# Kernel optimization log

Hardware: AMD Instinct MI355X
Metric: run time of the kernel (lower is better)

Reference implementation:

```python
import jax, jax.numpy as jnp
import numpy as np

N_NODES = 100_000
N_EDGES = 1_600_000
HID = 64
TXT = 384
N_LAYERS = 2
BATCH = 1024


def setup_inputs() -> dict:
    key = jax.random.key(0)
    ks = jax.random.split(key, 13)
    s = 0.05
    return {
        "text_emb": jax.random.normal(ks[0], (N_NODES, TXT), dtype=jnp.float32),
        "weights": jax.random.uniform(ks[1], (N_EDGES,), dtype=jnp.float32),
        "W_enc": jax.random.normal(ks[2], (TXT, HID), dtype=jnp.float32) * s,
        "b_enc": jax.random.normal(ks[3], (HID,), dtype=jnp.float32) * s,
        "Wself_f": jax.random.normal(ks[4], (N_LAYERS, HID, HID), dtype=jnp.float32) * s,
        "Wneigh_f": jax.random.normal(ks[5], (N_LAYERS, HID, HID), dtype=jnp.float32) * s,
        "b_f": jax.random.normal(ks[6], (N_LAYERS, HID), dtype=jnp.float32) * s,
        "Wself_r": jax.random.normal(ks[7], (N_LAYERS, HID, HID), dtype=jnp.float32) * s,
        "Wneigh_r": jax.random.normal(ks[8], (N_LAYERS, HID, HID), dtype=jnp.float32) * s,
        "b_r": jax.random.normal(ks[9], (N_LAYERS, HID), dtype=jnp.float32) * s,
        "src": jax.random.randint(ks[10], (N_EDGES,), 0, N_NODES, dtype=jnp.int32),
        "dst": jax.random.randint(ks[11], (N_EDGES,), 0, N_NODES, dtype=jnp.int32),
        "ids_idx": jax.random.randint(ks[12], (BATCH,), 0, N_NODES, dtype=jnp.int32),
    }


def _inv_degree(idx, n, e_dtype):
    deg = jax.ops.segment_sum(jnp.ones((idx.shape[0],), dtype=e_dtype), idx, num_segments=n)
    return jnp.where(deg > 0, 1.0 / deg, 0.0)  # zero in-degree -> 0 (DGL mean)


def _sage_mean(x, src, dst, w, inv_deg, Wself, Wneigh, b):
    # DGL SAGEConv('mean') with edge_weight: neigh = mean_over_in_edges(w * h_src)
    m = w[:, None] * x[src]                                   # [E, H] gather
    neigh = jax.ops.segment_sum(m, dst, num_segments=x.shape[0]) * inv_deg[:, None]
    return x @ Wself + neigh @ Wneigh + b


def reference(text_emb, weights, W_enc, b_enc, Wself_f, Wneigh_f, b_f,
              Wself_r, Wneigh_r, b_r, src, dst, ids_idx):
    n = text_emb.shape[0]
    inv_f = _inv_degree(dst, n, text_emb.dtype)   # forward graph: aggregate into dst
    inv_r = _inv_degree(src, n, text_emb.dtype)   # reversed graph: aggregate into src
    x = text_emb @ W_enc + b_enc                  # text encoder
    for l in range(Wself_f.shape[0]):
        y = jax.nn.relu(_sage_mean(x, src, dst, weights, inv_f,
                                   Wself_f[l], Wneigh_f[l], b_f[l]))
        y = y + jax.nn.relu(_sage_mean(x, dst, src, weights, inv_r,
                                       Wself_r[l], Wneigh_r[l], b_r[l]))
        x = x + y                                 # skip connection
    feat = x[ids_idx]                             # [B, H]
    return feat / jnp.linalg.norm(feat, axis=1, keepdims=True)
```

## Files before the change

### kernel.cpp

```cpp
#include <hip/hip_runtime.h>

#define NN 100000
#define NE 1600000
#define HID 64
#define TXT 384
#define BATCH 1024
#define NBUCK 391
#define SBLK 256
#define EPB ((NE + SBLK - 1) / SBLK)
#define LDA 40
#define LDK2 72

typedef __attribute__((ext_vector_type(8))) short short8;
typedef __attribute__((ext_vector_type(4))) float float4v;

__device__ __forceinline__ ushort f2bf(float f) {
  unsigned u = __float_as_uint(f);
  unsigned r = (u + 0x7fffu + ((u >> 16) & 1u)) >> 16;
  return (ushort)r;
}
__device__ __forceinline__ float bf2f(ushort u) {
  return __uint_as_float(((unsigned)u) << 16);
}
__device__ __forceinline__ short8 pack8(float4 a, float4 b) {
  short8 s;
  s[0] = (short)f2bf(a.x); s[1] = (short)f2bf(a.y);
  s[2] = (short)f2bf(a.z); s[3] = (short)f2bf(a.w);
  s[4] = (short)f2bf(b.x); s[5] = (short)f2bf(b.y);
  s[6] = (short)f2bf(b.z); s[7] = (short)f2bf(b.w);
  return s;
}

__global__ void k_hist2(const int* __restrict__ src, const int* __restrict__ dst,
                        int* __restrict__ cm_f, int* __restrict__ cm_r,
                        int* __restrict__ flagz) {
  __shared__ int hf[NBUCK], hr[NBUCK];
  const int t = threadIdx.x, blk = blockIdx.x;
  const int gid = blk * 256 + t;
  if (gid < NN / 4) flagz[gid] = 0;
  for (int i = t; i < NBUCK; i += 256) { hf[i] = 0; hr[i] = 0; }
  __syncthreads();
  const int e0 = blk * EPB, e1 = min(NE, e0 + EPB);
  for (int e = e0 + t; e < e1; e += 256) {
    atomicAdd(&hf[dst[e] >> 8], 1);
    atomicAdd(&hr[src[e] >> 8], 1);
  }
  __syncthreads();
  for (int i = t; i < NBUCK; i += 256) {
    cm_f[i * SBLK + blk] = hf[i];
    cm_r[i * SBLK + blk] = hr[i];
  }
}

__global__ void k_scan1(int* __restrict__ cm_f, int* __restrict__ cm_r,
                        int* __restrict__ btot) {
  __shared__ int tmp[256];
  const int t = threadIdx.x;
  int b = blockIdx.x;
  int* cm = (b < NBUCK) ? cm_f : cm_r;
  int bucket = (b < NBUCK) ? b : b - NBUCK;
  int* row = cm + bucket * SBLK;
  int v = row[t];
  tmp[t] = v; __syncthreads();
  for (int d = 1; d < 256; d <<= 1) {
    int s = tmp[t]; if (t >= d) s += tmp[t - d];
    __syncthreads(); tmp[t] = s; __syncthreads();
  }
  row[t] = tmp[t] - v;
  if (t == 255) btot[b] = tmp[t];
}

__global__ void k_scan2(const int* __restrict__ btot,
                        int* __restrict__ bbase_f, int* __restrict__ bbase_r) {
  __shared__ int tmp[512];
  const int t = threadIdx.x;
  int h = (t < NBUCK) ? btot[t] : 0;
  tmp[t] = h; __syncthreads();
  for (int d = 1; d < 512; d <<= 1) {
    int v = tmp[t]; if (t >= d) v += tmp[t - d];
    __syncthreads(); tmp[t] = v; __syncthreads();
  }
  if (t < NBUCK) bbase_f[t] = tmp[t] - h;
  __syncthreads();
  h = (t < NBUCK) ? btot[NBUCK + t] : 0;
  tmp[t] = h; __syncthreads();
  for (int d = 1; d < 512; d <<= 1) {
    int v = tmp[t]; if (t >= d) v += tmp[t - d];
    __syncthreads(); tmp[t] = v; __syncthreads();
  }
  if (t < NBUCK) bbase_r[t] = tmp[t] - h;
}

__global__ void k_scatter2(const int* __restrict__ src, const int* __restrict__ dst,
                           const float* __restrict__ w,
                           const int* __restrict__ cm_f, const int* __restrict__ cm_r,
                           const int* __restrict__ bbase_f, const int* __restrict__ bbase_r,
                           int2* __restrict__ stg_f, int2* __restrict__ stg_r) {
  __shared__ int cur_f[NBUCK], cur_r[NBUCK];
  const int t = threadIdx.x, blk = blockIdx.x;
  for (int i = t; i < NBUCK; i += 256) {
    cur_f[i] = bbase_f[i] + cm_f[i * SBLK + blk];
    cur_r[i] = bbase_r[i] + cm_r[i * SBLK + blk];
  }
  __syncthreads();
  const int e0 = blk * EPB, e1 = min(NE, e0 + EPB);
  for (int e = e0 + t; e < e1; e += 256) {
    int s = src[e], d = dst[e];
    int wb = __float_as_int(w[e]);
    int p = atomicAdd(&cur_f[d >> 8], 1);
    stg_f[p] = make_int2(((d & 255) << 24) | s, wb);
    int q = atomicAdd(&cur_r[s >> 8], 1);
    stg_r[q] = make_int2(((s & 255) << 24) | d, wb);
  }
}

__global__ void p_build(const int2* __restrict__ stgf, const int* __restrict__ btotf,
                        const int* __restrict__ bbasef,
                        int* __restrict__ startf, int* __restrict__ cntf,
                        int2* __restrict__ cvf, int* __restrict__ permf,
                        const int2* __restrict__ stgr, const int* __restrict__ btotr,
                        const int* __restrict__ bbaser,
                        int* __restrict__ startr, int* __restrict__ cntr,
                        int2* __restrict__ cvr, int* __restrict__ permr) {
  int b = blockIdx.x;
  const int2* stg; const int* bcnt; const int* bbase;
  int* start; int* cnt; int2* cv; int* perm;
  if (b < NBUCK) { stg = stgf; bcnt = btotf; bbase = bbasef; start = startf; cnt = cntf; cv = cvf; perm = permf; }
  else { b -= NBUCK; stg = stgr; bcnt = btotr; bbase = bbaser; start = startr; cnt = cntr; cv = cvr; perm = permr; }
  const int base = bbase[b];
  const int n = bcnt[b];
  const int t = threadIdx.x;
  __shared__ int hist[256], tmp[256], cur[256], dh[256], dc[256];
  hist[t] = 0;
  perm[b * 256 + t] = -1;
  __syncthreads();
  for (int i = t; i < n; i += 256) {
    unsigned pk = (unsigned)stg[base + i].x;
    atomicAdd(&hist[pk >> 24], 1);
  }
  __syncthreads();
  const int h = hist[t];
  tmp[t] = h; __syncthreads();
  for (int d = 1; d < 256; d <<= 1) {
    int v = tmp[t]; if (t >= d) v += tmp[t - d];
    __syncthreads(); tmp[t] = v; __syncthreads();
  }
  const int excl = tmp[t] - h;
  const int node = (b << 8) + t;
  const bool valid = (node < NN);
  if (valid) { start[node] = base + excl; cnt[node] = h; }
  cur[t] = excl;
  dh[t] = 0; __syncthreads();
  const int dcap = min(h, 255);
  if (valid) atomicAdd(&dh[dcap], 1);
  __syncthreads();
  int dv = dh[t];
  tmp[t] = dv; __syncthreads();
  for (int d = 1; d < 256; d <<= 1) {
    int v = tmp[t]; if (t >= d) v += tmp[t - d];
    __syncthreads(); tmp[t] = v; __syncthreads();
  }
  dc[t] = tmp[t] - dv;
  __syncthreads();
  if (valid) {
    int pos = atomicAdd(&dc[dcap], 1);
    perm[b * 256 + pos] = node;
  }
  __syncthreads();
  for (int i = t; i < n; i += 256) {
    int2 en = stg[base + i];
    unsigned d8 = ((unsigned)en.x) >> 24;
    int pos = atomicAdd(&cur[d8], 1);
    cv[base + pos] = make_int2(en.x & 0xFFFFFF, en.y);
  }
}

__global__ void k_flag(const int* __restrict__ ids,
                       const int* __restrict__ startf, const int* __restrict__ cntf,
                       const int2* __restrict__ cvf,
                       const int* __restrict__ startr, const int* __restrict__ cntr,
                       const int2* __restrict__ cvr,
                       unsigned char* __restrict__ flag) {
  int b = blockIdx.x * 256 + threadIdx.x;
  if (b >= BATCH) return;
  int row = ids[b];
  flag[row] = 1;
  int s = startf[row], e = s + cntf[row];
  for (int j = s; j < e; ++j) flag[cvf[j].x] = 1;
  s = startr[row]; e = s + cntr[row];
  for (int j = s; j < e; ++j) flag[cvr[j].x] = 1;
}

__global__ void k_gather3(const ushort* __restrict__ xb,
                          const unsigned char* __restrict__ flag,
                          const int* __restrict__ permf, const int* __restrict__ startf,
                          const int* __restrict__ cntf, const int2* __restrict__ cvf,
                          ushort* __restrict__ nbf,
                          const int* __restrict__ permr, const int* __restrict__ startr,
                          const int* __restrict__ cntr, const int2* __restrict__ cvr,
                          ushort* __restrict__ nbr) {
  const int BPD = (NBUCK * 256) / 16;
  int b = blockIdx.x;
  const int *perm, *start, *cnt; const int2* cv; ushort* outp;
  if (b < BPD) { perm = permf; start = startf; cnt = cntf; cv = cvf; outp = nbf; }
  else { b -= BPD; perm = permr; start = startr; cnt = cntr; cv = cvr; outp = nbr; }
  const int lane = threadIdx.x & 63;
  const int wave = threadIdx.x >> 6;
  const int slot = b * 16 + wave * 4 + (lane >> 4);
  const int fl = (lane & 15) * 4;
  const int row = perm[slot];
  if (row < 0) return;
  if (!flag[row]) return;
  const int s = start[row], c = cnt[row];
  const int e = s + c;
  float a0 = 0.f, a1 = 0.f, a2 = 0.f, a3 = 0.f;
  int j = s;
  for (; j + 4 <= e; j += 4) {
    int2 e0 = cv[j], e1 = cv[j + 1], e2 = cv[j + 2], e3 = cv[j + 3];
    uint2 v0 = *(const uint2*)(xb + (size_t)e0.x * 64 + fl);
    uint2 v1 = *(const uint2*)(xb + (size_t)e1.x * 64 + fl);
    uint2 v2 = *(const uint2*)(xb + (size_t)e2.x * 64 + fl);
    uint2 v3 = *(const uint2*)(xb + (size_t)e3.x * 64 + fl);
    float w0 = __int_as_float(e0.y), w1 = __int_as_float(e1.y);
    float w2 = __int_as_float(e2.y), w3 = __int_as_float(e3.y);
    a0 += w0 * bf2f((ushort)v0.x); a1 += w0 * bf2f((ushort)(v0.x >> 16));
    a2 += w0 * bf2f((ushort)v0.y); a3 += w0 * bf2f((ushort)(v0.y >> 16));
    a0 += w1 * bf2f((ushort)v1.x); a1 += w1 * bf2f((ushort)(v1.x >> 16));
    a2 += w1 * bf2f((ushort)v1.y); a3 += w1 * bf2f((ushort)(v1.y >> 16));
    a0 += w2 * bf2f((ushort)v2.x); a1 += w2 * bf2f((ushort)(v2.x >> 16));
    a2 += w2 * bf2f((ushort)v2.y); a3 += w2 * bf2f((ushort)(v2.y >> 16));
    a0 += w3 * bf2f((ushort)v3.x); a1 += w3 * bf2f((ushort)(v3.x >> 16));
    a2 += w3 * bf2f((ushort)v3.y); a3 += w3 * bf2f((ushort)(v3.y >> 16));
  }
  for (; j < e; ++j) {
    int2 ee = cv[j];
    uint2 v = *(const uint2*)(xb + (size_t)ee.x * 64 + fl);
    float ww = __int_as_float(ee.y);
    a0 += ww * bf2f((ushort)v.x); a1 += ww * bf2f((ushort)(v.x >> 16));
    a2 += ww * bf2f((ushort)v.y); a3 += ww * bf2f((ushort)(v.y >> 16));
  }
  float inv = (c > 0) ? 1.0f / (float)c : 0.f;
  uint2 pv;
  pv.x = (uint)f2bf(a0 * inv) | ((uint)f2bf(a1 * inv) << 16);
  pv.y = (uint)f2bf(a2 * inv) | ((uint)f2bf(a3 * inv) << 16);
  *(uint2*)(outp + (size_t)row * 64 + fl) = pv;
}

__global__ void k_bgather(const ushort* __restrict__ xb, const int* __restrict__ ids,
                          const int* __restrict__ startf, const int* __restrict__ cntf,
                          const int2* __restrict__ cvf, ushort* __restrict__ nbf,
                          const int* __restrict__ startr, const int* __restrict__ cntr,
                          const int2* __restrict__ cvr, ushort* __restrict__ nbr) {
  const int lane = threadIdx.x & 63;
  const int wave = threadIdx.x >> 6;
  const int fl = (lane & 15) * 4;
  const int t = blockIdx.x * 16 + wave * 4 + (lane >> 4);
  const int rev = (t >= BATCH);
  const int b = rev ? t - BATCH : t;
  const int row = ids[b];
  const int* start = rev ? startr : startf;
  const int* cnt   = rev ? cntr   : cntf;
  const int2* cv   = rev ? cvr    : cvf;
  ushort* outp     = rev ? nbr    : nbf;
  const int s = start[row], c = cnt[row];
  const int e = s + c;
  float a0 = 0.f, a1 = 0.f, a2 = 0.f, a3 = 0.f;
  int j = s;
  for (; j + 4 <= e; j += 4) {
    int2 e0 = cv[j], e1 = cv[j + 1], e2 = cv[j + 2], e3 = cv[j + 3];
    uint2 v0 = *(const uint2*)(xb + (size_t)e0.x * 64 + fl);
    uint2 v1 = *(const uint2*)(xb + (size_t)e1.x * 64 + fl);
    uint2 v2 = *(const uint2*)(xb + (size_t)e2.x * 64 + fl);
    uint2 v3 = *(const uint2*)(xb + (size_t)e3.x * 64 + fl);
    float w0 = __int_as_float(e0.y), w1 = __int_as_float(e1.y);
    float w2 = __int_as_float(e2.y), w3 = __int_as_float(e3.y);
    a0 += w0 * bf2f((ushort)v0.x); a1 += w0 * bf2f((ushort)(v0.x >> 16));
    a2 += w0 * bf2f((ushort)v0.y); a3 += w0 * bf2f((ushort)(v0.y >> 16));
    a0 += w1 * bf2f((ushort)v1.x); a1 += w1 * bf2f((ushort)(v1.x >> 16));
    a2 += w1 * bf2f((ushort)v1.y); a3 += w1 * bf2f((ushort)(v1.y >> 16));
    a0 += w2 * bf2f((ushort)v2.x); a1 += w2 * bf2f((ushort)(v2.x >> 16));
    a2 += w2 * bf2f((ushort)v2.y); a3 += w2 * bf2f((ushort)(v2.y >> 16));
    a0 += w3 * bf2f((ushort)v3.x); a1 += w3 * bf2f((ushort)(v3.x >> 16));
    a2 += w3 * bf2f((ushort)v3.y); a3 += w3 * bf2f((ushort)(v3.y >> 16));
  }
  for (; j < e; ++j) {
    int2 ee = cv[j];
    uint2 v = *(const uint2*)(xb + (size_t)ee.x * 64 + fl);
    float ww = __int_as_float(ee.y);
    a0 += ww * bf2f((ushort)v.x); a1 += ww * bf2f((ushort)(v.x >> 16));
    a2 += ww * bf2f((ushort)v.y); a3 += ww * bf2f((ushort)(v.y >> 16));
  }
  float inv = (c > 0) ? 1.0f / (float)c : 0.f;
  uint2 pv;
  pv.x = (uint)f2bf(a0 * inv) | ((uint)f2bf(a1 * inv) << 16);
  pv.y = (uint)f2bf(a2 * inv) | ((uint)f2bf(a3 * inv) << 16);
  *(uint2*)(outp + (size_t)b * 64 + fl) = pv;
}

__global__ void k_wtile(const float* __restrict__ W, ushort* __restrict__ Wt) {
  int b = blockIdx.x;
  int ch = b >> 2, nt = b & 3;
  int lane = threadIdx.x;
  int quad = lane >> 4, lr = lane & 15;
  short8 s;
  #pragma unroll
  for (int j = 0; j < 8; ++j)
    s[j] = (short)f2bf(W[(ch * 32 + quad * 8 + j) * 64 + nt * 16 + lr]);
  *(short8*)&Wt[((size_t)b * 64 + lane) * 8] = s;
}

__launch_bounds__(256)
__global__ void k_enc3(const float* __restrict__ T, const ushort* __restrict__ Wt,
                       const float* __restrict__ bias,
                       float* __restrict__ x, ushort* __restrict__ xb) {
  __shared__ short As[2][128 * LDA];
  const int tid = threadIdx.x;
  const int row0 = blockIdx.x * 128;
  const int wave = tid >> 6, lane = tid & 63;
  const int quad = lane >> 4, lr = lane & 15;
  const int srow = tid >> 1, shalf = (tid & 1) * 16;
  const int grow = min(row0 + srow, NN - 1);
  const float* tp = T + (size_t)grow * TXT + shalf;

  float4 pa0 = *(const float4*)(tp);
  float4 pa1 = *(const float4*)(tp + 4);
  float4 pa2 = *(const float4*)(tp + 8);
  float4 pa3 = *(const float4*)(tp + 12);
  *(short8*)&As[0][srow * LDA + shalf] = pack8(pa0, pa1);
  *(short8*)&As[0][srow * LDA + shalf + 8] = pack8(pa2, pa3);
  pa0 = *(const float4*)(tp + 32);
  pa1 = *(const float4*)(tp + 36);
  pa2 = *(const float4*)(tp + 40);
  pa3 = *(const float4*)(tp + 44);
  __syncthreads();

  const ushort* pw = Wt + lane * 8;
  float4v acc[2][4] = {};
  #pragma unroll
  for (int ch = 0; ch < 12; ++ch) {
    const short* Ac = As[ch & 1];
    short8 af0 = *(const short8*)&Ac[(wave * 32 + lr) * LDA + quad * 8];
    short8 af1 = *(const short8*)&Ac[(wave * 32 + 16 + lr) * LDA + quad * 8];
    #pragma unroll
    for (int nt = 0; nt < 4; ++nt) {
      short8 bfrag = *(const short8*)(pw + (size_t)(ch * 4 + nt) * 512);
      acc[0][nt] = __builtin_amdgcn_mfma_f32_16x16x32_bf16(af0, bfrag, acc[0][nt], 0, 0, 0);
      acc[1][nt] = __builtin_amdgcn_mfma_f32_16x16x32_bf16(af1, bfrag, acc[1][nt], 0, 0, 0);
    }
    if (ch < 11) {
      short* An = As[(ch + 1) & 1];
      *(short8*)&An[srow * LDA + shalf] = pack8(pa0, pa1);
      *(short8*)&An[srow * LDA + shalf + 8] = pack8(pa2, pa3);
      if (ch + 2 < 12) {
        const float* q = tp + (ch + 2) * 32;
        pa0 = *(const float4*)(q);
        pa1 = *(const float4*)(q + 4);
        pa2 = *(const float4*)(q + 8);
        pa3 = *(const float4*)(q + 12);
      }
      __syncthreads();
    }
  }
  #pragma unroll
  for (int nt = 0; nt < 4; ++nt) {
    const int col = nt * 16 + lr;
    const float bcol = bias[col];
    #pragma unroll
    for (int mt = 0; mt < 2; ++mt) {
      #pragma unroll
      for (int r = 0; r < 4; ++r) {
        const int row = row0 + wave * 32 + mt * 16 + quad * 4 + r;
        if (row < NN) {
          float v = acc[mt][nt][r] + bcol;
          x[(size_t)row * 64 + col] = v;
          xb[(size_t)row * 64 + col] = f2bf(v);
        }
      }
    }
  }
}

__launch_bounds__(256)
__global__ void k_layer(const ushort* __restrict__ xbin,
                        const ushort* __restrict__ nbf, const ushort* __restrict__ nbr,
                        const float* __restrict__ Wsf, const float* __restrict__ Wnf,
                        const float* __restrict__ bfv,
                        const float* __restrict__ Wsr, const float* __restrict__ Wnr,
                        const float* __restrict__ brv,
                        float* __restrict__ x, ushort* __restrict__ xb) {
  __shared__ short B4[4 * 64 * LDK2];
  __shared__ short As[128 * LDK2];
  const int tid = threadIdx.x;
  const int row0 = blockIdx.x * 128;
  const int wave = tid >> 6, lane = tid & 63;
  const int quad = lane >> 4, lr = lane & 15;

  {
    const float* wm0 = Wsf; const float* wm1 = Wsr;
    const float* wm2 = Wnf; const float* wm3 = Wnr;
    #pragma unroll
    for (int j = 0; j < 16; ++j) {
      int idx = j * 256 + tid;
      int k = idx >> 6, n = idx & 63;
      B4[0 * 64 * LDK2 + n * LDK2 + k] = (short)f2bf(wm0[idx]);
      B4[1 * 64 * LDK2 + n * LDK2 + k] = (short)f2bf(wm1[idx]);
      B4[2 * 64 * LDK2 + n * LDK2 + k] = (short)f2bf(wm2[idx]);
      B4[3 * 64 * LDK2 + n * LDK2 + k] = (short)f2bf(wm3[idx]);
    }
  }
  const int srow = tid >> 1, half = (tid & 1) * 32;
  const int grow = min(row0 + srow, NN - 1);
  {
    const uint4* s = (const uint4*)(xbin + (size_t)grow * 64 + half);
    uint4* d = (uint4*)&As[srow * LDK2 + half];
    d[0] = s[0]; d[1] = s[1]; d[2] = s[2]; d[3] = s[3];
  }
  const uint4* pf = (const uint4*)(nbf + (size_t)grow * 64 + half);
  uint4 p0 = pf[0], p1 = pf[1], p2 = pf[2], p3 = pf[3];
  __syncthreads();

  float4v accf[2][4] = {}, accr[2][4] = {};
  #pragma unroll
  for (int kk = 0; kk < 64; kk += 32) {
    short8 a0 = *(const short8*)&As[(wave * 32 + lr) * LDK2 + kk + quad * 8];
    short8 a1 = *(const short8*)&As[(wave * 32 + 16 + lr) * LDK2 + kk + quad * 8];
    #pragma unroll
    for (int nt = 0; nt < 4; ++nt) {
      short8 bs = *(const short8*)&B4[0 * 64 * LDK2 + (nt * 16 + lr) * LDK2 + kk + quad * 8];
      accf[0][nt] = __builtin_amdgcn_mfma_f32_16x16x32_bf16(a0, bs, accf[0][nt], 0, 0, 0);
      accf[1][nt] = __builtin_amdgcn_mfma_f32_16x16x32_bf16(a1, bs, accf[1][nt], 0, 0, 0);
      short8 bq = *(const short8*)&B4[1 * 64 * LDK2 + (nt * 16 + lr) * LDK2 + kk + quad * 8];
      accr[0][nt] = __builtin_amdgcn_mfma_f32_16x16x32_bf16(a0, bq, accr[0][nt], 0, 0, 0);
      accr[1][nt] = __builtin_amdgcn_mfma_f32_16x16x32_bf16(a1, bq, accr[1][nt], 0, 0, 0);
    }
  }
  __syncthreads();
  { uint4* d = (uint4*)&As[srow * LDK2 + half]; d[0] = p0; d[1] = p1; d[2] = p2; d[3] = p3; }
  {
    const uint4* pr = (const uint4*)(nbr + (size_t)grow * 64 + half);
    p0 = pr[0]; p1 = pr[1]; p2 = pr[2]; p3 = pr[3];
  }
  __syncthreads();
  #pragma unroll
  for (int kk = 0; kk < 64; kk += 32) {
    short8 a0 = *(const short8*)&As[(wave * 32 + lr) * LDK2 + kk + quad * 8];
    short8 a1 = *(const short8*)&As[(wave * 32 + 16 + lr) * LDK2 + kk + quad * 8];
    #pragma unroll
    for (int nt = 0; nt < 4; ++nt) {
      short8 bs = *(const short8*)&B4[2 * 64 * LDK2 + (nt * 16 + lr) * LDK2 + kk + quad * 8];
      accf[0][nt] = __builtin_amdgcn_mfma_f32_16x16x32_bf16(a0, bs, accf[0][nt], 0, 0, 0);
      accf[1][nt] = __builtin_amdgcn_mfma_f32_16x16x32_bf16(a1, bs, accf[1][nt], 0, 0, 0);
    }
  }
  __syncthreads();
  { uint4* d = (uint4*)&As[srow * LDK2 + half]; d[0] = p0; d[1] = p1; d[2] = p2; d[3] = p3; }
  __syncthreads();
  #pragma unroll
  for (int kk = 0; kk < 64; kk += 32) {
    short8 a0 = *(const short8*)&As[(wave * 32 + lr) * LDK2 + kk + quad * 8];
    short8 a1 = *(const short8*)&As[(wave * 32 + 16 + lr) * LDK2 + kk + quad * 8];
    #pragma unroll
    for (int nt = 0; nt < 4; ++nt) {
      short8 bs = *(const short8*)&B4[3 * 64 * LDK2 + (nt * 16 + lr) * LDK2 + kk + quad * 8];
      accr[0][nt] = __builtin_amdgcn_mfma_f32_16x16x32_bf16(a0, bs, accr[0][nt], 0, 0, 0);
      accr[1][nt] = __builtin_amdgcn_mfma_f32_16x16x32_bf16(a1, bs, accr[1][nt], 0, 0, 0);
    }
  }
  #pragma unroll
  for (int nt = 0; nt < 4; ++nt) {
    const int col = nt * 16 + lr;
    const float bf_c = bfv[col], br_c = brv[col];
    #pragma unroll
    for (int mt = 0; mt < 2; ++mt) {
      #pragma unroll
      for (int r = 0; r < 4; ++r) {
        const int row = row0 + wave * 32 + mt * 16 + quad * 4 + r;
        if (row < NN) {
          size_t idx = (size_t)row * 64 + col;
          float v = x[idx] + fmaxf(accf[mt][nt][r] + bf_c, 0.f)
                           + fmaxf(accr[mt][nt][r] + br_c, 0.f);
          x[idx] = v;
          xb[idx] = f2bf(v);
        }
      }
    }
  }
}

__launch_bounds__(256)
__global__ void k_blayer(const ushort* __restrict__ xbin, const float* __restrict__ x,
                         const int* __restrict__ ids,
                         const ushort* __restrict__ nbf, const ushort* __restrict__ nbr,
                         const float* __restrict__ Wsf, const float* __restrict__ Wnf,
                         const float* __restrict__ bfv,
                         const float* __restrict__ Wsr, const float* __restrict__ Wnr,
                         const float* __restrict__ brv,
                         float* __restrict__ out) {
  __shared__ short B4[4 * 64 * LDK2];
  __shared__ short As[128 * LDK2];
  const int tid = threadIdx.x;
  const int b0 = blockIdx.x * 128;
  const int wave = tid >> 6, lane = tid & 63;
  const int quad = lane >> 4, lr = lane & 15;

  #pragma unroll
  for (int j = 0; j < 16; ++j) {
    int idx = j * 256 + tid;
    int k = idx >> 6, n = idx & 63;
    B4[0 * 64 * LDK2 + n * LDK2 + k] = (short)f2bf(Wsf[idx]);
    B4[1 * 64 * LDK2 + n * LDK2 + k] = (short)f2bf(Wsr[idx]);
    B4[2 * 64 * LDK2 + n * LDK2 + k] = (short)f2bf(Wnf[idx]);
    B4[3 * 64 * LDK2 + n * LDK2 + k] = (short)f2bf(Wnr[idx]);
  }
  const int srow = tid >> 1, half = (tid & 1) * 32;
  const int node0 = ids[b0 + srow];
  {
    const uint4* s = (const uint4*)(xbin + (size_t)node0 * 64 + half);
    uint4* d = (uint4*)&As[srow * LDK2 + half];
    d[0] = s[0]; d[1] = s[1]; d[2] = s[2]; d[3] = s[3];
  }
  __syncthreads();

  float4v accf[2][4] = {}, accr[2][4] = {};
  #pragma unroll
  for (int kk = 0; kk < 64; kk += 32) {
    short8 a0 = *(const short8*)&As[(wave * 32 + lr) * LDK2 + kk + quad * 8];
    short8 a1 = *(const short8*)&As[(wave * 32 + 16 + lr) * LDK2 + kk + quad * 8];
    #pragma unroll
    for (int nt = 0; nt < 4; ++nt) {
      short8 bs = *(const short8*)&B4[0 * 64 * LDK2 + (nt * 16 + lr) * LDK2 + kk + quad * 8];
      accf[0][nt] = __builtin_amdgcn_mfma_f32_16x16x32_bf16(a0, bs, accf[0][nt], 0, 0, 0);
      accf[1][nt] = __builtin_amdgcn_mfma_f32_16x16x32_bf16(a1, bs, accf[1][nt], 0, 0, 0);
      short8 bq = *(const short8*)&B4[1 * 64 * LDK2 + (nt * 16 + lr) * LDK2 + kk + quad * 8];
      accr[0][nt] = __builtin_amdgcn_mfma_f32_16x16x32_bf16(a0, bq, accr[0][nt], 0, 0, 0);
      accr[1][nt] = __builtin_amdgcn_mfma_f32_16x16x32_bf16(a1, bq, accr[1][nt], 0, 0, 0);
    }
  }
  __syncthreads();
  {
    const uint4* s = (const uint4*)(nbf + (size_t)(b0 + srow) * 64 + half);
    uint4* d = (uint4*)&As[srow * LDK2 + half];
    d[0] = s[0]; d[1] = s[1]; d[2] = s[2]; d[3] = s[3];
  }
  __syncthreads();
  #pragma unroll
  for (int kk = 0; kk < 64; kk += 32) {
    short8 a0 = *(const short8*)&As[(wave * 32 + lr) * LDK2 + kk + quad * 8];
    short8 a1 = *(const short8*)&As[(wave * 32 + 16 + lr) * LDK2 + kk + quad * 8];
    #pragma unroll
    for (int nt = 0; nt < 4; ++nt) {
      short8 bs = *(const short8*)&B4[2 * 64 * LDK2 + (nt * 16 + lr) * LDK2 + kk + quad * 8];
      accf[0][nt] = __builtin_amdgcn_mfma_f32_16x16x32_bf16(a0, bs, accf[0][nt], 0, 0, 0);
      accf[1][nt] = __builtin_amdgcn_mfma_f32_16x16x32_bf16(a1, bs, accf[1][nt], 0, 0, 0);
    }
  }
  __syncthreads();
  {
    const uint4* s = (const uint4*)(nbr + (size_t)(b0 + srow) * 64 + half);
    uint4* d = (uint4*)&As[srow * LDK2 + half];
    d[0] = s[0]; d[1] = s[1]; d[2] = s[2]; d[3] = s[3];
  }
  __syncthreads();
  #pragma unroll
  for (int kk = 0; kk < 64; kk += 32) {
    short8 a0 = *(const short8*)&As[(wave * 32 + lr) * LDK2 + kk + quad * 8];
    short8 a1 = *(const short8*)&As[(wave * 32 + 16 + lr) * LDK2 + kk + quad * 8];
    #pragma unroll
    for (int nt = 0; nt < 4; ++nt) {
      short8 bs = *(const short8*)&B4[3 * 64 * LDK2 + (nt * 16 + lr) * LDK2 + kk + quad * 8];
      accr[0][nt] = __builtin_amdgcn_mfma_f32_16x16x32_bf16(a0, bs, accr[0][nt], 0, 0, 0);
      accr[1][nt] = __builtin_amdgcn_mfma_f32_16x16x32_bf16(a1, bs, accr[1][nt], 0, 0, 0);
    }
  }
  float vv[2][4][4];
  #pragma unroll
  for (int nt = 0; nt < 4; ++nt) {
    const int col = nt * 16 + lr;
    const float bf_c = bfv[col], br_c = brv[col];
    #pragma unroll
    for (int mt = 0; mt < 2; ++mt) {
      #pragma unroll
      for (int r = 0; r < 4; ++r) {
        const int rl = wave * 32 + mt * 16 + quad * 4 + r;
        const int node = ids[b0 + rl];
        vv[mt][nt][r] = x[(size_t)node * 64 + col]
                      + fmaxf(accf[mt][nt][r] + bf_c, 0.f)
                      + fmaxf(accr[mt][nt][r] + br_c, 0.f);
      }
    }
  }
  #pragma unroll
  for (int mt = 0; mt < 2; ++mt) {
    #pragma unroll
    for (int r = 0; r < 4; ++r) {
      float s = 0.f;
      #pragma unroll
      for (int nt = 0; nt < 4; ++nt) s += vv[mt][nt][r] * vv[mt][nt][r];
      s += __shfl_xor(s, 1); s += __shfl_xor(s, 2);
      s += __shfl_xor(s, 4); s += __shfl_xor(s, 8);
      const int rl = wave * 32 + mt * 16 + quad * 4 + r;
      const float inv = 1.f / sqrtf(s);
      #pragma unroll
      for (int nt = 0; nt < 4; ++nt)
        out[(size_t)(b0 + rl) * 64 + nt * 16 + lr] = vv[mt][nt][r] * inv;
    }
  }
}

extern "C" void kernel_launch(void* const* d_in, const int* in_sizes, int n_in,
                              void* d_out, int out_size, void* d_ws, size_t ws_size,
                              hipStream_t stream) {
  const float* text = (const float*)d_in[0];
  const float* wts  = (const float*)d_in[1];
  const float* Wenc = (const float*)d_in[2];
  const float* benc = (const float*)d_in[3];
  const float* Wsf  = (const float*)d_in[4];
  const float* Wnf  = (const float*)d_in[5];
  const float* bf   = (const float*)d_in[6];
  const float* Wsr  = (const float*)d_in[7];
  const float* Wnr  = (const float*)d_in[8];
  const float* br   = (const float*)d_in[9];
  const int*   src  = (const int*)d_in[10];
  const int*   dst  = (const int*)d_in[11];
  const int*   ids  = (const int*)d_in[12];
  float* out = (float*)d_out;

  char* ws = (char*)d_ws;
  size_t o = 0;
  auto alloc = [&](size_t f32elems) {
    void* p = ws + o;
    o += f32elems * 4;
    o = (o + 255) & ~(size_t)255;
    return p;
  };
  float*  x   = (float*)alloc((size_t)NN * 64);
  ushort* xb  = (ushort*)alloc((size_t)NN * 32);
  ushort* nbf = (ushort*)alloc((size_t)NN * 32);
  ushort* nbr = (ushort*)alloc((size_t)NN * 32);
  ushort* Wt  = (ushort*)alloc(48 * 512 / 2);
  int2*   cvf = (int2*)alloc((size_t)NE * 2);
  int2*   cvr = (int2*)alloc((size_t)NE * 2);
  int* cm_f    = (int*)alloc((size_t)NBUCK * SBLK);
  int* cm_r    = (int*)alloc((size_t)NBUCK * SBLK);
  int* btot    = (int*)alloc(2 * NBUCK);
  int* bbase_f = (int*)alloc(NBUCK);
  int* bbase_r = (int*)alloc(NBUCK);
  int* startf  = (int*)alloc(NN);
  int* cntf    = (int*)alloc(NN);
  int* startr  = (int*)alloc(NN);
  int* cntr    = (int*)alloc(NN);
  int* permf   = (int*)alloc((size_t)NBUCK * 256);
  int* permr   = (int*)alloc((size_t)NBUCK * 256);
  unsigned char* flag = (unsigned char*)alloc(NN / 4 + 64);

  int2* stg_f = (int2*)nbf;
  int2* stg_r = (int2*)nbr;

  const int EB2 = (NN + 127) / 128;

  k_wtile<<<48, 64, 0, stream>>>(Wenc, Wt);
  k_hist2<<<SBLK, 256, 0, stream>>>(src, dst, cm_f, cm_r, (int*)flag);
  k_scan1<<<2 * NBUCK, 256, 0, stream>>>(cm_f, cm_r, btot);
  k_scan2<<<1, 512, 0, stream>>>(btot, bbase_f, bbase_r);
  k_scatter2<<<SBLK, 256, 0, stream>>>(src, dst, wts, cm_f, cm_r,
                                       bbase_f, bbase_r, stg_f, stg_r);
  p_build<<<2 * NBUCK, 256, 0, stream>>>(stg_f, btot, bbase_f, startf, cntf, cvf, permf,
                                         stg_r, btot + NBUCK, bbase_r, startr, cntr, cvr, permr);
  k_flag<<<BATCH / 256, 256, 0, stream>>>(ids, startf, cntf, cvf, startr, cntr, cvr, flag);
  k_enc3<<<EB2, 256, 0, stream>>>(text, Wt, benc, x, xb);

  const int GB3 = 2 * ((NBUCK * 256) / 16);
  k_gather3<<<GB3, 256, 0, stream>>>(xb, flag, permf, startf, cntf, cvf, nbf,
                                     permr, startr, cntr, cvr, nbr);
  k_layer<<<EB2, 256, 0, stream>>>(xb, nbf, nbr,
                                   Wsf, Wnf, bf, Wsr, Wnr, br, x, xb);
  k_bgather<<<(2 * BATCH) / 16, 256, 0, stream>>>(xb, ids, startf, cntf, cvf, nbf,
                                                  startr, cntr, cvr, nbr);
  k_blayer<<<BATCH / 128, 256, 0, stream>>>(xb, x, ids, nbf, nbr,
                                            Wsf + HID * HID, Wnf + HID * HID, bf + HID,
                                            Wsr + HID * HID, Wnr + HID * HID, br + HID,
                                            out);
}
```

Baseline: 517.4 us.

## Prune CSR build and layer-1 work to the batch's one-hop neighbourhood

Computes the set of flagged nodes (batch nodes plus their in- and out-neighbours) up front with an extra pass over the edges. That set then filters the histogram, the scatter and the per-node CSR build, so only edges into flagged nodes are bucketed. The flagged rows are compacted into a list, and the first SAGE layer runs its MFMA update only over those rows instead of all nodes. This cuts scatter traffic and layer-1 compute, in exchange for an extra edge sweep with random byte lookups, an atomic compaction step, and indirect row indexing in the layer kernel.

```diff
diff --git a/kernel.cpp b/kernel.cpp
--- a/kernel.cpp
+++ b/kernel.cpp
@@ -31,19 +31,50 @@
   return s;
 }
 
+__global__ void k_clear(unsigned char* __restrict__ idmap,
+                        unsigned char* __restrict__ flag, int* __restrict__ nf) {
+  int i = blockIdx.x * 256 + threadIdx.x;
+  if (i < NN) { idmap[i] = 0; flag[i] = 0; }
+  if (i == 0) *nf = 0;
+}
+
+__global__ void k_seed(const int* __restrict__ ids,
+                       unsigned char* __restrict__ idmap,
+                       unsigned char* __restrict__ flag) {
+  int b = blockIdx.x * 256 + threadIdx.x;
+  if (b < BATCH) { int r = ids[b]; idmap[r] = 1; flag[r] = 1; }
+}
+
+__global__ void k_fedges(const int* __restrict__ src, const int* __restrict__ dst,
+                         const unsigned char* __restrict__ idmap,
+                         unsigned char* __restrict__ flag) {
+  const int t = threadIdx.x, blk = blockIdx.x;
+  const int e0 = blk * EPB, e1 = min(NE, e0 + EPB);
+  for (int e = e0 + t; e < e1; e += 256) {
+    int s = src[e], d = dst[e];
+    if (idmap[d]) flag[s] = 1;
+    if (idmap[s]) flag[d] = 1;
+  }
+}
+
+__global__ void k_compact(const unsigned char* __restrict__ flag,
+                          int* __restrict__ frows, int* __restrict__ nf) {
+  int i = blockIdx.x * 256 + threadIdx.x;
+  if (i < NN && flag[i]) frows[atomicAdd(nf, 1)] = i;
+}
+
 __global__ void k_hist2(const int* __restrict__ src, const int* __restrict__ dst,
-                        int* __restrict__ cm_f, int* __restrict__ cm_r,
-                        int* __restrict__ flagz) {
+                        const unsigned char* __restrict__ flag,
+                        int* __restrict__ cm_f, int* __restrict__ cm_r) {
   __shared__ int hf[NBUCK], hr[NBUCK];
   const int t = threadIdx.x, blk = blockIdx.x;
-  const int gid = blk * 256 + t;
-  if (gid < NN / 4) flagz[gid] = 0;
   for (int i = t; i < NBUCK; i += 256) { hf[i] = 0; hr[i] = 0; }
   __syncthreads();
   const int e0 = blk * EPB, e1 = min(NE, e0 + EPB);
   for (int e = e0 + t; e < e1; e += 256) {
-    atomicAdd(&hf[dst[e] >> 8], 1);
-    atomicAdd(&hr[src[e] >> 8], 1);
+    int s = src[e], d = dst[e];
+    if (flag[d]) atomicAdd(&hf[d >> 8], 1);
+    if (flag[s]) atomicAdd(&hr[s >> 8], 1);
   }
   __syncthreads();
   for (int i = t; i < NBUCK; i += 256) {
@@ -93,6 +124,7 @@
 
 __global__ void k_scatter2(const int* __restrict__ src, const int* __restrict__ dst,
                            const float* __restrict__ w,
+                           const unsigned char* __restrict__ flag,
                            const int* __restrict__ cm_f, const int* __restrict__ cm_r,
                            const int* __restrict__ bbase_f, const int* __restrict__ bbase_r,
                            int2* __restrict__ stg_f, int2* __restrict__ stg_r) {
@@ -107,14 +139,19 @@
   for (int e = e0 + t; e < e1; e += 256) {
     int s = src[e], d = dst[e];
     int wb = __float_as_int(w[e]);
-    int p = atomicAdd(&cur_f[d >> 8], 1);
-    stg_f[p] = make_int2(((d & 255) << 24) | s, wb);
-    int q = atomicAdd(&cur_r[s >> 8], 1);
-    stg_r[q] = make_int2(((s & 255) << 24) | d, wb);
-  }
-}
-
-__global__ void p_build(const int2* __restrict__ stgf, const int* __restrict__ btotf,
+    if (flag[d]) {
+      int p = atomicAdd(&cur_f[d >> 8], 1);
+      stg_f[p] = make_int2(((d & 255) << 24) | s, wb);
+    }
+    if (flag[s]) {
+      int q = atomicAdd(&cur_r[s >> 8], 1);
+      stg_r[q] = make_int2(((s & 255) << 24) | d, wb);
+    }
+  }
+}
+
+__global__ void p_build(const unsigned char* __restrict__ flag,
+                        const int2* __restrict__ stgf, const int* __restrict__ btotf,
                         const int* __restrict__ bbasef,
                         int* __restrict__ startf, int* __restrict__ cntf,
                         int2* __restrict__ cvf, int* __restrict__ permf,
@@ -147,7 +184,7 @@
   }
   const int excl = tmp[t] - h;
   const int node = (b << 8) + t;
-  const bool valid = (node < NN);
+  const bool valid = (node < NN) && flag[node];
   if (valid) { start[node] = base + excl; cnt[node] = h; }
   cur[t] = excl;
   dh[t] = 0; __syncthreads();
@@ -175,24 +212,7 @@
   }
 }
 
-__global__ void k_flag(const int* __restrict__ ids,
-                       const int* __restrict__ startf, const int* __restrict__ cntf,
-                       const int2* __restrict__ cvf,
-                       const int* __restrict__ startr, const int* __restrict__ cntr,
-                       const int2* __restrict__ cvr,
-                       unsigned char* __restrict__ flag) {
-  int b = blockIdx.x * 256 + threadIdx.x;
-  if (b >= BATCH) return;
-  int row = ids[b];
-  flag[row] = 1;
-  int s = startf[row], e = s + cntf[row];
-  for (int j = s; j < e; ++j) flag[cvf[j].x] = 1;
-  s = startr[row]; e = s + cntr[row];
-  for (int j = s; j < e; ++j) flag[cvr[j].x] = 1;
-}
-
 __global__ void k_gather3(const ushort* __restrict__ xb,
-                          const unsigned char* __restrict__ flag,
                           const int* __restrict__ permf, const int* __restrict__ startf,
                           const int* __restrict__ cntf, const int2* __restrict__ cvf,
                           ushort* __restrict__ nbf,
@@ -210,7 +230,6 @@
   const int fl = (lane & 15) * 4;
   const int row = perm[slot];
   if (row < 0) return;
-  if (!flag[row]) return;
   const int s = start[row], c = cnt[row];
   const int e = s + c;
   float a0 = 0.f, a1 = 0.f, a2 = 0.f, a3 = 0.f;
@@ -381,35 +400,37 @@
 }
 
 __launch_bounds__(256)
-__global__ void k_layer(const ushort* __restrict__ xbin,
-                        const ushort* __restrict__ nbf, const ushort* __restrict__ nbr,
-                        const float* __restrict__ Wsf, const float* __restrict__ Wnf,
-                        const float* __restrict__ bfv,
-                        const float* __restrict__ Wsr, const float* __restrict__ Wnr,
-                        const float* __restrict__ brv,
-                        float* __restrict__ x, ushort* __restrict__ xb) {
+__global__ void k_layerf(const int* __restrict__ frows, const int* __restrict__ nfp,
+                         const ushort* __restrict__ xbin,
+                         const ushort* __restrict__ nbf, const ushort* __restrict__ nbr,
+                         const float* __restrict__ Wsf, const float* __restrict__ Wnf,
+                         const float* __restrict__ bfv,
+                         const float* __restrict__ Wsr, const float* __restrict__ Wnr,
+                         const float* __restrict__ brv,
+                         float* __restrict__ x, ushort* __restrict__ xb) {
+  const int nfv = *nfp;
+  const int row0 = blockIdx.x * 128;
+  if (row0 >= nfv) return;
   __shared__ short B4[4 * 64 * LDK2];
   __shared__ short As[128 * LDK2];
   const int tid = threadIdx.x;
-  const int row0 = blockIdx.x * 128;
   const int wave = tid >> 6, lane = tid & 63;
   const int quad = lane >> 4, lr = lane & 15;
 
   {
-    const float* wm0 = Wsf; const float* wm1 = Wsr;
-    const float* wm2 = Wnf; const float* wm3 = Wnr;
     #pragma unroll
     for (int j = 0; j < 16; ++j) {
       int idx = j * 256 + tid;
       int k = idx >> 6, n = idx & 63;
-      B4[0 * 64 * LDK2 + n * LDK2 + k] = (short)f2bf(wm0[idx]);
-      B4[1 * 64 * LDK2 + n * LDK2 + k] = (short)f2bf(wm1[idx]);
-      B4[2 * 64 * LDK2 + n * LDK2 + k] = (short)f2bf(wm2[idx]);
-      B4[3 * 64 * LDK2 + n * LDK2 + k] = (short)f2bf(wm3[idx]);
+      B4[0 * 64 * LDK2 + n * LDK2 + k] = (short)f2bf(Wsf[idx]);
+      B4[1 * 64 * LDK2 + n * LDK2 + k] = (short)f2bf(Wsr[idx]);
+      B4[2 * 64 * LDK2 + n * LDK2 + k] = (short)f2bf(Wnf[idx]);
+      B4[3 * 64 * LDK2 + n * LDK2 + k] = (short)f2bf(Wnr[idx]);
     }
   }
   const int srow = tid >> 1, half = (tid & 1) * 32;
-  const int grow = min(row0 + srow, NN - 1);
+  const int slot = row0 + srow;
+  const int grow = frows[(slot < nfv) ? slot : 0];
   {
     const uint4* s = (const uint4*)(xbin + (size_t)grow * 64 + half);
     uint4* d = (uint4*)&As[srow * LDK2 + half];
@@ -474,9 +495,11 @@
     for (int mt = 0; mt < 2; ++mt) {
       #pragma unroll
       for (int r = 0; r < 4; ++r) {
-        const int row = row0 + wave * 32 + mt * 16 + quad * 4 + r;
-        if (row < NN) {
-          size_t idx = (size_t)row * 64 + col;
+        const int rl = wave * 32 + mt * 16 + quad * 4 + r;
+        const int slotE = row0 + rl;
+        if (slotE < nfv) {
+          const int node = frows[slotE];
+          size_t idx = (size_t)node * 64 + col;
           float v = x[idx] + fmaxf(accf[mt][nt][r] + bf_c, 0.f)
                            + fmaxf(accr[mt][nt][r] + br_c, 0.f);
           x[idx] = v;
@@ -651,7 +674,10 @@
   int* cntr    = (int*)alloc(NN);
   int* permf   = (int*)alloc((size_t)NBUCK * 256);
   int* permr   = (int*)alloc((size_t)NBUCK * 256);
-  unsigned char* flag = (unsigned char*)alloc(NN / 4 + 64);
+  unsigned char* idmap = (unsigned char*)alloc(NN / 4 + 64);
+  unsigned char* flag  = (unsigned char*)alloc(NN / 4 + 64);
+  int* frows = (int*)alloc(NN);
+  int* nf    = (int*)alloc(64);
 
   int2* stg_f = (int2*)nbf;
   int2* stg_r = (int2*)nbr;
@@ -659,21 +685,25 @@
   const int EB2 = (NN + 127) / 128;
 
   k_wtile<<<48, 64, 0, stream>>>(Wenc, Wt);
-  k_hist2<<<SBLK, 256, 0, stream>>>(src, dst, cm_f, cm_r, (int*)flag);
+  k_clear<<<NBUCK, 256, 0, stream>>>(idmap, flag, nf);
+  k_seed<<<(BATCH + 255) / 256, 256, 0, stream>>>(ids, idmap, flag);
+  k_fedges<<<SBLK, 256, 0, stream>>>(src, dst, idmap, flag);
+  k_hist2<<<SBLK, 256, 0, stream>>>(src, dst, flag, cm_f, cm_r);
   k_scan1<<<2 * NBUCK, 256, 0, stream>>>(cm_f, cm_r, btot);
   k_scan2<<<1, 512, 0, stream>>>(btot, bbase_f, bbase_r);
-  k_scatter2<<<SBLK, 256, 0, stream>>>(src, dst, wts, cm_f, cm_r,
+  k_scatter2<<<SBLK, 256, 0, stream>>>(src, dst, wts, flag, cm_f, cm_r,
                                        bbase_f, bbase_r, stg_f, stg_r);
-  p_build<<<2 * NBUCK, 256, 0, stream>>>(stg_f, btot, bbase_f, startf, cntf, cvf, permf,
+  p_build<<<2 * NBUCK, 256, 0, stream>>>(flag,
+                                         stg_f, btot, bbase_f, startf, cntf, cvf, permf,
                                          stg_r, btot + NBUCK, bbase_r, startr, cntr, cvr, permr);
-  k_flag<<<BATCH / 256, 256, 0, stream>>>(ids, startf, cntf, cvf, startr, cntr, cvr, flag);
+  k_compact<<<NBUCK, 256, 0, stream>>>(flag, frows, nf);
   k_enc3<<<EB2, 256, 0, stream>>>(text, Wt, benc, x, xb);
 
   const int GB3 = 2 * ((NBUCK * 256) / 16);
-  k_gather3<<<GB3, 256, 0, stream>>>(xb, flag, permf, startf, cntf, cvf, nbf,
+  k_gather3<<<GB3, 256, 0, stream>>>(xb, permf, startf, cntf, cvf, nbf,
                                      permr, startr, cntr, cvr, nbr);
-  k_layer<<<EB2, 256, 0, stream>>>(xb, nbf, nbr,
-                                   Wsf, Wnf, bf, Wsr, Wnr, br, x, xb);
+  k_layerf<<<EB2, 256, 0, stream>>>(frows, nf, xb, nbf, nbr,
+                                    Wsf, Wnf, bf, Wsr, Wnr, br, x, xb);
   k_bgather<<<(2 * BATCH) / 16, 256, 0, stream>>>(xb, ids, startf, cntf, cvf, nbf,
                                                   startr, cntr, cvr, nbr);
   k_blayer<<<BATCH / 128, 256, 0, stream>>>(xb, x, ids, nbf, nbr,
```

Result: faster. 482.3 us (-6.8%).
